# Kernel tuning notes

Hardware: AMD Instinct MI355X
Metric: run time of the kernel (lower is better)

The kernel has to match this reference:

```python
import jax, jax.numpy as jnp
import numpy as np

V, BLK, H, D, L = 32000, 1024, 16, 1024, 3
HD = D // H  # 64
B, T = 4, 1024


def _layernorm(x, g, b, eps=1e-5):
    mu = jnp.mean(x, axis=-1, keepdims=True)
    var = jnp.mean(jnp.square(x - mu), axis=-1, keepdims=True)
    return (x - mu) * jax.lax.rsqrt(var + eps) * g + b


def setup_inputs() -> dict:
    key = jax.random.key(0)
    ks = jax.random.split(key, 32)
    s = 0.02
    inp = {}
    inp["idx"] = jax.random.randint(ks[0], (B, T), 0, V)
    inp["target"] = jax.random.randint(ks[1], (B, T), 0, V)
    inp["tok_emb"] = jax.random.normal(ks[2], (V, D), jnp.float32) * s
    inp["pos_emb"] = jax.random.normal(ks[3], (BLK, D), jnp.float32) * s
    inp["wq"] = jax.random.normal(ks[4], (L, H, D, HD), jnp.float32) * s
    inp["wk"] = jax.random.normal(ks[5], (L, H, D, HD), jnp.float32) * s
    inp["wv"] = jax.random.normal(ks[6], (L, H, D, HD), jnp.float32) * s
    inp["wproj"] = jax.random.normal(ks[7], (L, D, D), jnp.float32) * s
    inp["bproj"] = jnp.zeros((L, D), jnp.float32)
    inp["ln1_g"] = jnp.ones((L, D), jnp.float32)
    inp["ln1_b"] = jnp.zeros((L, D), jnp.float32)
    inp["ln2_g"] = jnp.ones((L, D), jnp.float32)
    inp["ln2_b"] = jnp.zeros((L, D), jnp.float32)
    inp["w1"] = jax.random.normal(ks[8], (L, D, 4 * D), jnp.float32) * s
    inp["b1"] = jnp.zeros((L, 4 * D), jnp.float32)
    inp["w2"] = jax.random.normal(ks[9], (L, 4 * D, D), jnp.float32) * s
    inp["b2"] = jnp.zeros((L, D), jnp.float32)
    inp["lnf_g"] = jnp.ones((D,), jnp.float32)
    inp["lnf_b"] = jnp.zeros((D,), jnp.float32)
    inp["wlm"] = jax.random.normal(ks[10], (D, V), jnp.float32) * s
    inp["blm"] = jnp.zeros((V,), jnp.float32)
    return inp


def reference(idx, target, tok_emb, pos_emb, wq, wk, wv, wproj, bproj,
              ln1_g, ln1_b, ln2_g, ln2_b, w1, b1, w2, b2,
              lnf_g, lnf_b, wlm, blm):
    Bb, Tt = idx.shape
    x = tok_emb[idx] + pos_emb[:Tt]  # [B,T,D]
    mask = jnp.tril(jnp.ones((Tt, Tt), dtype=bool))  # causal
    scale = D ** -0.5  # NOTE: source scales by n_embd**-0.5, not head_size**-0.5
    for l in range(L):
        xn = _layernorm(x, ln1_g[l], ln1_b[l])
        q = jnp.einsum('btd,hde->bhte', xn, wq[l])
        k = jnp.einsum('btd,hde->bhte', xn, wk[l])
        v = jnp.einsum('btd,hde->bhte', xn, wv[l])
        scores = jnp.einsum('bhte,bhse->bhts', q, k) * scale
        scores = jnp.where(mask, scores, -jnp.inf)
        attn = jax.nn.softmax(scores, axis=-1)
        o = jnp.einsum('bhts,bhse->bhte', attn, v)
        o = o.transpose(0, 2, 1, 3).reshape(Bb, Tt, D)  # concat heads
        x = x + o @ wproj[l] + bproj[l]
        xn2 = _layernorm(x, ln2_g[l], ln2_b[l])
        h = jax.nn.relu(xn2 @ w1[l] + b1[l])
        x = x + h @ w2[l] + b2[l]
    x = _layernorm(x, lnf_g, lnf_b)
    logits = x @ wlm + blm  # [B,T,V]
    logp = jax.nn.log_softmax(logits, axis=-1)
    nll = -jnp.take_along_axis(logp, target[..., None], axis=-1)[..., 0]
    loss = jnp.mean(nll)
    return logits, loss
```

## Files before the change

kernel.cpp:

```cpp
#include <hip/hip_runtime.h>
#include <math.h>

#define Dn   1024
#define Hn   16
#define HDn  64
#define Tn   1024
#define Bn   4
#define Vn   32000
#define Ln   3
#define NT   (Bn*Tn)

typedef __attribute__((ext_vector_type(8))) short bf16x8;
typedef __attribute__((ext_vector_type(4))) float f32x4;

__device__ __forceinline__ float b2f(unsigned short u) {
  union { float f; unsigned int i; } c; c.i = ((unsigned int)u) << 16; return c.f;
}
__device__ __forceinline__ unsigned short f2b(float f) {
  union { float f; unsigned int i; } c; c.f = f;
  unsigned int r = (c.i + 0x7FFFu + ((c.i >> 16) & 1u)) >> 16;
  return (unsigned short)r;
}

#define GLOAD_LDS16(g, l) __builtin_amdgcn_global_load_lds( \
    (const __attribute__((address_space(1))) void*)(g),     \
    (__attribute__((address_space(3))) void*)(l), 16, 0, 0)

#define SBAR()  __builtin_amdgcn_s_barrier()
#define SCHED() __builtin_amdgcn_sched_barrier(0)

__device__ __forceinline__ void xcd_swz(int& bx, int& by) {
  int gx = gridDim.x, nwg = gx * gridDim.y;
  int lin = by * gx + bx;
  int swz = (lin & 7) * (nwg >> 3) + (lin >> 3);
  bx = swz % gx; by = swz / gx;
}

__global__ __launch_bounds__(256) void embed_kernel(
    const int* __restrict__ idx, const float* __restrict__ tok,
    const float* __restrict__ pos, float* __restrict__ x) {
  int row = blockIdx.x;
  int t = row & (Tn - 1);
  int token = idx[row];
  const float4* tp = (const float4*)(tok + (size_t)token * Dn);
  const float4* pp = (const float4*)(pos + (size_t)t * Dn);
  float4* xp = (float4*)(x + (size_t)row * Dn);
  int i = threadIdx.x;
  float4 a = tp[i], b = pp[i];
  xp[i] = make_float4(a.x + b.x, a.y + b.y, a.z + b.z, a.w + b.w);
}

__global__ __launch_bounds__(256) void ln_kernel(
    const float* __restrict__ x, const float* __restrict__ g,
    const float* __restrict__ b, unsigned short* __restrict__ y) {
  int row = blockIdx.x;
  const float4* xr = (const float4*)(x + (size_t)row * Dn);
  __shared__ float red[4];
  int lane = threadIdx.x & 63, w = threadIdx.x >> 6;

  float4 v = xr[threadIdx.x];
  float s = v.x + v.y + v.z + v.w;
  #pragma unroll
  for (int o = 32; o > 0; o >>= 1) s += __shfl_down(s, o, 64);
  if (lane == 0) red[w] = s;
  __syncthreads();
  float mu = (red[0] + red[1] + red[2] + red[3]) * (1.0f / Dn);
  __syncthreads();

  float dx = v.x - mu, dy = v.y - mu, dz = v.z - mu, dw = v.w - mu;
  float ss = dx*dx + dy*dy + dz*dz + dw*dw;
  #pragma unroll
  for (int o = 32; o > 0; o >>= 1) ss += __shfl_down(ss, o, 64);
  if (lane == 0) red[w] = ss;
  __syncthreads();
  float var = (red[0] + red[1] + red[2] + red[3]) * (1.0f / Dn);
  float inv = rsqrtf(var + 1e-5f);

  float4 gv = ((const float4*)g)[threadIdx.x];
  float4 bv = ((const float4*)b)[threadIdx.x];
  ushort4 o4;
  o4.x = f2b(dx*inv*gv.x + bv.x);
  o4.y = f2b(dy*inv*gv.y + bv.y);
  o4.z = f2b(dz*inv*gv.z + bv.z);
  o4.w = f2b(dw*inv*gv.w + bv.w);
  ((ushort4*)(y + (size_t)row * Dn))[threadIdx.x] = o4;
}

__global__ __launch_bounds__(256) void wcast_kernel(
    const float* __restrict__ src, unsigned short* __restrict__ dst,
    int K, int M, long long bsk, long long bsh) {
  __shared__ float t[32][33];
  int m0 = blockIdx.x << 5, k0 = blockIdx.y << 5;
  int tid = threadIdx.x;
  int ml = tid & 31, kl = tid >> 5;
  #pragma unroll
  for (int p = 0; p < 4; ++p) {
    int k = k0 + kl + p * 8;
    int m = m0 + ml;
    t[ml][kl + p * 8] = src[(size_t)k * bsk + (size_t)(m >> 6) * bsh + (m & 63)];
  }
  __syncthreads();
  int kl2 = tid & 31, ml2 = tid >> 5;
  #pragma unroll
  for (int p = 0; p < 4; ++p) {
    int m = m0 + ml2 + p * 8;
    int k = k0 + kl2;
    dst[(size_t)m * K + k] = f2b(t[ml2 + p * 8][kl2]);
  }
}

__global__ __launch_bounds__(256) void wcast3_kernel(
    const float* __restrict__ s0, const float* __restrict__ s1,
    const float* __restrict__ s2, unsigned short* __restrict__ dst) {
  const float* src = (blockIdx.z == 0) ? s0 : (blockIdx.z == 1) ? s1 : s2;
  unsigned short* d = dst + (size_t)blockIdx.z * 1024 * Dn;
  __shared__ float t[32][33];
  int m0 = blockIdx.x << 5, k0 = blockIdx.y << 5;
  int tid = threadIdx.x;
  int ml = tid & 31, kl = tid >> 5;
  #pragma unroll
  for (int p = 0; p < 4; ++p) {
    int k = k0 + kl + p * 8;
    int m = m0 + ml;
    t[ml][kl + p * 8] = src[(size_t)k * HDn + (size_t)(m >> 6) * (Dn * HDn) + (m & 63)];
  }
  __syncthreads();
  int kl2 = tid & 31, ml2 = tid >> 5;
  #pragma unroll
  for (int p = 0; p < 4; ++p) {
    int m = m0 + ml2 + p * 8;
    int k = k0 + kl2;
    d[(size_t)m * Dn + k] = f2b(t[ml2 + p * 8][kl2]);
  }
}

__global__ __launch_bounds__(512) void mm_bf16(
    const unsigned short* __restrict__ A, const unsigned short* __restrict__ BT,
    const float* __restrict__ bias, const float* __restrict__ res,
    float* __restrict__ Cf, unsigned short* __restrict__ Ch,
    int N, int K, int M, int relu) {
  __shared__ __align__(16) unsigned short As[3][128 * 32];
  __shared__ __align__(16) unsigned short Bs[3][128 * 32];
  const int tid = threadIdx.x;
  const int lane = tid & 63, w = tid >> 6, g = lane >> 4;
  const int wr = w >> 2, wc = w & 3;
  int bx = blockIdx.x, by = blockIdx.y;
  xcd_swz(bx, by);
  const int n0 = bx << 7, m0 = by << 7;

  f32x4 acc[4][2];
  #pragma unroll
  for (int i = 0; i < 4; ++i)
    #pragma unroll
    for (int j = 0; j < 2; ++j)
      acc[i][j] = (f32x4){0.f, 0.f, 0.f, 0.f};

  const int srow = tid >> 2, su = tid & 3;
  const int sks = su ^ ((srow >> 1) & 3);
  const unsigned short* a_g = A + (size_t)(n0 + srow) * K + sks * 8;
  const unsigned short* b_g = BT + (size_t)(m0 + srow) * K + sks * 8;

  int a_off[4], b_off[2];
  #pragma unroll
  for (int f = 0; f < 4; ++f) {
    int row = wr * 64 + f * 16 + (lane & 15);
    a_off[f] = row * 64 + ((g ^ ((row >> 1) & 3)) << 4);
  }
  #pragma unroll
  for (int f = 0; f < 2; ++f) {
    int col = wc * 32 + f * 16 + (lane & 15);
    b_off[f] = col * 64 + ((g ^ ((col >> 1) & 3)) << 4);
  }

#define MM_STAGE(buf, kk) do {                                   \
    GLOAD_LDS16(a_g + (kk), As[buf] + tid * 8);                  \
    GLOAD_LDS16(b_g + (kk), Bs[buf] + tid * 8); } while (0)

#define MM_COMPUTE(buf) do {                                     \
    bf16x8 af[4], bfr[2];                                        \
    _Pragma("unroll")                                            \
    for (int f = 0; f < 4; ++f)                                  \
      af[f] = *(const bf16x8*)((const char*)As[buf] + a_off[f]); \
    _Pragma("unroll")                                            \
    for (int f = 0; f < 2; ++f)                                  \
      bfr[f] = *(const bf16x8*)((const char*)Bs[buf] + b_off[f]);\
    _Pragma("unroll")                                            \
    for (int i = 0; i < 4; ++i)                                  \
      _Pragma("unroll")                                          \
      for (int j = 0; j < 2; ++j)                                \
        acc[i][j] = __builtin_amdgcn_mfma_f32_16x16x32_bf16(af[i], bfr[j], acc[i][j], 0, 0, 0); } while (0)

  MM_STAGE(0, 0);
  MM_STAGE(1, 32);
  int bc = 0, bp = 2;
  for (int k0 = 0; k0 < K; k0 += 32) {
    if (k0 + 32 < K) asm volatile("s_waitcnt vmcnt(2)" ::: "memory");
    else             asm volatile("s_waitcnt vmcnt(0)" ::: "memory");
    SCHED(); SBAR(); SCHED();
    if (k0 + 64 < K) MM_STAGE(bp, k0 + 64);
    MM_COMPUTE(bc);
    bc = (bc == 2) ? 0 : bc + 1;
    bp = (bp == 2) ? 0 : bp + 1;
  }

  #pragma unroll
  for (int fc = 0; fc < 2; ++fc) {
    int colg = m0 + wc * 32 + fc * 16 + (lane & 15);
    float bz = bias ? bias[colg] : 0.f;
    #pragma unroll
    for (int fr = 0; fr < 4; ++fr) {
      #pragma unroll
      for (int i = 0; i < 4; ++i) {
        int rowg = n0 + wr * 64 + fr * 16 + (g << 2) + i;
        float v = acc[fr][fc][i] + bz;
        if (res) v += res[(size_t)rowg * M + colg];
        if (relu) v = fmaxf(v, 0.f);
        if (Cf) Cf[(size_t)rowg * M + colg] = v;
        else    Ch[(size_t)rowg * M + colg] = f2b(v);
      }
    }
  }
#undef MM_STAGE
#undef MM_COMPUTE
}

template<int OMODE>
__global__ __launch_bounds__(512, 2) void mm256_bf16(
    const unsigned short* __restrict__ A, const unsigned short* __restrict__ BT,
    const float* __restrict__ bias, const float* __restrict__ res,
    float* __restrict__ Cf, unsigned short* __restrict__ Ch,
    float* __restrict__ rowsum, int N, int K, int M, int relu) {
  __shared__ __align__(16) unsigned short As[2][256 * 64];
  __shared__ __align__(16) unsigned short Bs[2][256 * 64];
  __shared__ float rsum2[OMODE == 4 ? 256 * 4 : 4];
  const int tid = threadIdx.x;
  const int lane = tid & 63, w = tid >> 6, g = lane >> 4;
  const int wr = w >> 2, wc = w & 3;
  int bx = blockIdx.x, by = blockIdx.y;
  xcd_swz(bx, by);
  const int n0 = bx << 8, m0 = by << 8;

  f32x4 acc[8][4];
  #pragma unroll
  for (int i = 0; i < 8; ++i)
    #pragma unroll
    for (int j = 0; j < 4; ++j)
      acc[i][j] = (f32x4){0.f, 0.f, 0.f, 0.f};

  const unsigned short* ag[4];
  const unsigned short* bg[4];
  int lofs[4];
  #pragma unroll
  for (int j = 0; j < 4; ++j) {
    int c = tid + 512 * j;
    int row = c >> 3, u = c & 7;
    int ks = u ^ (row & 7);
    ag[j] = A + (size_t)(n0 + row) * K + ks * 8;
    bg[j] = BT + (size_t)(m0 + row) * K + ks * 8;
    lofs[j] = c * 8;
  }

  int aoff[2][2][4], boff[2][2][2];
  #pragma unroll
  for (int h0 = 0; h0 < 2; ++h0)
    #pragma unroll
    for (int ks = 0; ks < 2; ++ks) {
      #pragma unroll
      for (int fr = 0; fr < 4; ++fr) {
        int r = wr * 128 + h0 * 64 + fr * 16 + (lane & 15);
        aoff[h0][ks][fr] = r * 128 + (((g + ks * 4) ^ (r & 7)) << 4);
      }
      #pragma unroll
      for (int fb = 0; fb < 2; ++fb) {
        int cB = wc * 64 + ks * 32 + fb * 16 + (lane & 15);
        (void)cB;
      }
    }
  #pragma unroll
  for (int h1 = 0; h1 < 2; ++h1)
    #pragma unroll
    for (int ks = 0; ks < 2; ++ks)
      #pragma unroll
      for (int fb = 0; fb < 2; ++fb) {
        int cB = wc * 64 + h1 * 32 + fb * 16 + (lane & 15);
        boff[h1][ks][fb] = cB * 128 + (((g + ks * 4) ^ (cB & 7)) << 4);
      }

  #pragma unroll
  for (int j = 0; j < 4; ++j) {
    GLOAD_LDS16(ag[j], As[0] + lofs[j]);
    GLOAD_LDS16(bg[j], Bs[0] + lofs[j]);
  }
  asm volatile("s_waitcnt vmcnt(0)" ::: "memory");
  SCHED(); SBAR(); SCHED();

  int cur = 0;
  const int NKT = K >> 6;
  for (int kt = 0; kt < NKT; ++kt) {
    if (kt + 1 < NKT) {
      const int kn = (kt + 1) << 6;
      #pragma unroll
      for (int j = 0; j < 4; ++j) {
        GLOAD_LDS16(ag[j] + kn, As[cur ^ 1] + lofs[j]);
        GLOAD_LDS16(bg[j] + kn, Bs[cur ^ 1] + lofs[j]);
      }
    }
    const char* Ab = (const char*)As[cur];
    const char* Bb = (const char*)Bs[cur];
    #pragma unroll
    for (int h0 = 0; h0 < 2; ++h0) {
      #pragma unroll
      for (int ks = 0; ks < 2; ++ks) {
        bf16x8 af[4];
        #pragma unroll
        for (int fr = 0; fr < 4; ++fr)
          af[fr] = *(const bf16x8*)(Ab + aoff[h0][ks][fr]);
        #pragma unroll
        for (int h1 = 0; h1 < 2; ++h1) {
          bf16x8 b0 = *(const bf16x8*)(Bb + boff[h1][ks][0]);
          bf16x8 b1 = *(const bf16x8*)(Bb + boff[h1][ks][1]);
          #pragma unroll
          for (int fr = 0; fr < 4; ++fr) {
            acc[h0 * 4 + fr][h1 * 2 + 0] =
                __builtin_amdgcn_mfma_f32_16x16x32_bf16(af[fr], b0, acc[h0 * 4 + fr][h1 * 2 + 0], 0, 0, 0);
            acc[h0 * 4 + fr][h1 * 2 + 1] =
                __builtin_amdgcn_mfma_f32_16x16x32_bf16(af[fr], b1, acc[h0 * 4 + fr][h1 * 2 + 1], 0, 0, 0);
          }
        }
      }
    }
    asm volatile("s_waitcnt vmcnt(0)" ::: "memory");
    SCHED(); SBAR(); SCHED();
    cur ^= 1;
  }

  if (OMODE == 0) {
    #pragma unroll
    for (int fc = 0; fc < 4; ++fc) {
      int colg = m0 + wc * 64 + fc * 16 + (lane & 15);
      float bz = bias ? bias[colg] : 0.f;
      #pragma unroll
      for (int fr = 0; fr < 8; ++fr) {
        #pragma unroll
        for (int i = 0; i < 4; ++i) {
          int rowg = n0 + wr * 128 + fr * 16 + (g << 2) + i;
          float v = acc[fr][fc][i] + bz;
          if (res) v += res[(size_t)rowg * M + colg];
          if (relu) v = fmaxf(v, 0.f);
          if (Cf) Cf[(size_t)rowg * M + colg] = v;
          else    Ch[(size_t)rowg * M + colg] = f2b(v);
        }
      }
    }
  } else if (OMODE == 3) {
    unsigned short* kb  = Ch + (size_t)NT * Dn;
    unsigned short* vtb = Ch + 2 * (size_t)NT * Dn;
    #pragma unroll
    for (int fc = 0; fc < 4; ++fc) {
      int colg = m0 + wc * 64 + fc * 16 + (lane & 15);
      int sel = colg >> 10, hh = (colg >> 6) & 15, e = colg & 63;
      #pragma unroll
      for (int fr = 0; fr < 8; ++fr) {
        int rowg0 = n0 + wr * 128 + fr * 16 + (g << 2);
        int b = rowg0 >> 10, t0 = rowg0 & 1023;
        if (sel == 2) {
          ushort4 pk;
          pk.x = f2b(acc[fr][fc][0]); pk.y = f2b(acc[fr][fc][1]);
          pk.z = f2b(acc[fr][fc][2]); pk.w = f2b(acc[fr][fc][3]);
          *(ushort4*)&vtb[(((size_t)(b * 16 + hh) * 64) + e) * 1024 + t0] = pk;
        } else {
          unsigned short* dst = (sel == 0) ? Ch : kb;
          #pragma unroll
          for (int i = 0; i < 4; ++i)
            dst[(((size_t)(b * 16 + hh) * 1024) + t0 + i) * 64 + e] = f2b(acc[fr][fc][i]);
        }
      }
    }
  } else {
    #pragma unroll
    for (int fr = 0; fr < 8; ++fr) {
      #pragma unroll
      for (int i = 0; i < 4; ++i) {
        int rloc = wr * 128 + fr * 16 + (g << 2) + i;
        int rowg = n0 + rloc;
        float es = 0.f;
        #pragma unroll
        for (int fc = 0; fc < 4; ++fc) {
          int colg = m0 + wc * 64 + fc * 16 + (lane & 15);
          float v = acc[fr][fc][i] + bias[colg];
          __builtin_nontemporal_store(v, &Cf[(size_t)rowg * M + colg]);
          es += __expf(v);
        }
        es += __shfl_xor(es, 1); es += __shfl_xor(es, 2);
        es += __shfl_xor(es, 4); es += __shfl_xor(es, 8);
        if ((lane & 15) == 0) rsum2[rloc * 4 + wc] = es;
      }
    }
    __syncthreads();
    if (tid < 256)
      atomicAdd(&rowsum[n0 + tid],
                rsum2[tid * 4 + 0] + rsum2[tid * 4 + 1] +
                rsum2[tid * 4 + 2] + rsum2[tid * 4 + 3]);
  }
}

__global__ __launch_bounds__(256) void fattn_kernel(
    const unsigned short* __restrict__ qg, const unsigned short* __restrict__ kg,
    const unsigned short* __restrict__ vtg, unsigned short* __restrict__ ob) {
  const int bid = blockIdx.x;
  const int qt = bid & 15, bh = bid >> 4;
  const int b = bh >> 4, h = bh & 15;
  const int tid = threadIdx.x, lane = tid & 63, w = tid >> 6, g = lane >> 4;

  __shared__ __align__(16) unsigned short Ks[2][64 * 64];
  __shared__ __align__(16) unsigned short Vs[2][64 * 64];
  __shared__ __align__(16) unsigned short Pb[4][16 * 64];

  const unsigned short* kbase = kg + (size_t)bh * Tn * HDn;
  const unsigned short* vbase = vtg + (size_t)bh * HDn * Tn;

  const int qrow = qt * 64 + w * 16 + (lane & 15);
  const unsigned short* qptr = qg + ((size_t)bh * Tn + qrow) * HDn;
  bf16x8 qf0 = *(const bf16x8*)(qptr + g * 8);
  bf16x8 qf1 = *(const bf16x8*)(qptr + 32 + g * 8);

  f32x4 accO[4];
  #pragma unroll
  for (int dt = 0; dt < 4; ++dt) accO[dt] = (f32x4){0.f, 0.f, 0.f, 0.f};
  float mrun[4] = {-1e30f, -1e30f, -1e30f, -1e30f};
  float lrun[4] = {0.f, 0.f, 0.f, 0.f};

  const float scale = 0.03125f;
  const int qout0 = qt * 64 + w * 16 + 4 * g;

  unsigned short* pb = &Pb[w][0];
  const int nsteps = qt + 1;

#define FA_STAGE(buf, s0_) do {                                              \
    _Pragma("unroll")                                                        \
    for (int r = 0; r < 2; ++r) {                                            \
      int c = tid + 256 * r;                                                 \
      int srow = c >> 3, u = c & 7;                                          \
      GLOAD_LDS16(kbase + (size_t)((s0_) + srow) * HDn + ((u ^ (srow & 7)) * 8), Ks[buf] + c * 8); \
    }                                                                        \
    _Pragma("unroll")                                                        \
    for (int r = 0; r < 2; ++r) {                                            \
      int c = tid + 256 * r;                                                 \
      int d = c >> 3, u = c & 7;                                             \
      GLOAD_LDS16(vbase + (size_t)d * Tn + (s0_) + ((u ^ (d & 7)) * 8), Vs[buf] + c * 8); \
    } } while (0)

  FA_STAGE(0, 0);
  int cur = 0;

  for (int st = 0; st < nsteps; ++st) {
    const int s0 = st * 64;
    if (st + 1 < nsteps) {
      FA_STAGE(cur ^ 1, s0 + 64);
      asm volatile("s_waitcnt vmcnt(4)" ::: "memory");
    } else {
      asm volatile("s_waitcnt vmcnt(0)" ::: "memory");
    }
    SCHED(); SBAR(); SCHED();

    float p[4][4];
    #pragma unroll
    for (int sub = 0; sub < 4; ++sub) {
      int srow = sub * 16 + (lane & 15);
      const char* kr = (const char*)Ks[cur] + srow * 128;
      bf16x8 kf0 = *(const bf16x8*)(kr + ((g ^ (srow & 7)) * 16));
      bf16x8 kf1 = *(const bf16x8*)(kr + (((4 + g) ^ (srow & 7)) * 16));
      f32x4 s4 = (f32x4){0.f, 0.f, 0.f, 0.f};
      s4 = __builtin_amdgcn_mfma_f32_16x16x32_bf16(qf0, kf0, s4, 0, 0, 0);
      s4 = __builtin_amdgcn_mfma_f32_16x16x32_bf16(qf1, kf1, s4, 0, 0, 0);
      int sg = s0 + srow;
      #pragma unroll
      for (int i = 0; i < 4; ++i)
        p[sub][i] = (sg > qout0 + i) ? -1e30f : s4[i] * scale;
    }

    #pragma unroll
    for (int i = 0; i < 4; ++i) {
      float v = fmaxf(fmaxf(p[0][i], p[1][i]), fmaxf(p[2][i], p[3][i]));
      v = fmaxf(v, __shfl_xor(v, 1)); v = fmaxf(v, __shfl_xor(v, 2));
      v = fmaxf(v, __shfl_xor(v, 4)); v = fmaxf(v, __shfl_xor(v, 8));
      float nm = fmaxf(mrun[i], v);
      float fac = __expf(mrun[i] - nm);
      mrun[i] = nm;
      #pragma unroll
      for (int dt = 0; dt < 4; ++dt) accO[dt][i] *= fac;
      float sum = 0.f;
      #pragma unroll
      for (int sub = 0; sub < 4; ++sub) {
        float e = __expf(p[sub][i] - nm);
        p[sub][i] = e;
        sum += e;
      }
      sum += __shfl_xor(sum, 1); sum += __shfl_xor(sum, 2);
      sum += __shfl_xor(sum, 4); sum += __shfl_xor(sum, 8);
      lrun[i] = lrun[i] * fac + sum;
    }

    #pragma unroll
    for (int sub = 0; sub < 4; ++sub) {
      int s = sub * 16 + (lane & 15);
      #pragma unroll
      for (int i = 0; i < 4; ++i) {
        int q = 4 * g + i;
        pb[q * 64 + (((s >> 3) ^ (q & 7)) * 8) + (s & 7)] = f2b(p[sub][i]);
      }
    }

    #pragma unroll
    for (int sc = 0; sc < 2; ++sc) {
      int qq = lane & 15;
      bf16x8 pa = *(const bf16x8*)((const char*)pb + qq * 128 + (((sc * 4 + g) ^ (qq & 7)) * 16));
      #pragma unroll
      for (int dt = 0; dt < 4; ++dt) {
        int d = dt * 16 + (lane & 15);
        bf16x8 vf = *(const bf16x8*)((const char*)Vs[cur] + d * 128 + (((sc * 4 + g) ^ (d & 7)) * 16));
        accO[dt] = __builtin_amdgcn_mfma_f32_16x16x32_bf16(pa, vf, accO[dt], 0, 0, 0);
      }
    }

    SCHED(); SBAR(); SCHED();
    cur ^= 1;
  }
#undef FA_STAGE

  float rinv[4];
  #pragma unroll
  for (int i = 0; i < 4; ++i) rinv[i] = 1.0f / lrun[i];
  #pragma unroll
  for (int dt = 0; dt < 4; ++dt) {
    int dcol = h * 64 + dt * 16 + (lane & 15);
    #pragma unroll
    for (int i = 0; i < 4; ++i) {
      int t = qout0 + i;
      ob[((size_t)(b * Tn + t)) * Dn + dcol] = f2b(accO[dt][i] * rinv[i]);
    }
  }
}

__global__ __launch_bounds__(256) void loss_kernel(
    const float* __restrict__ logits, const float* __restrict__ rowsum,
    const int* __restrict__ target, float* __restrict__ out_loss) {
  __shared__ float red[4];
  int lane = threadIdx.x & 63, w = threadIdx.x >> 6;
  float s = 0.f;
  for (int row = threadIdx.x; row < NT; row += 256) {
    float lt = logits[(size_t)row * Vn + target[row]];
    s += logf(rowsum[row]) - lt;
  }
  #pragma unroll
  for (int off = 32; off > 0; off >>= 1) s += __shfl_down(s, off, 64);
  if (lane == 0) red[w] = s;
  __syncthreads();
  if (threadIdx.x == 0)
    *out_loss = (red[0] + red[1] + red[2] + red[3]) * (1.0f / NT);
}

static inline void launch_wcast(const float* src, unsigned short* dst, int K, int M,
                                long long bsk, long long bsh, hipStream_t s) {
  dim3 g(M >> 5, K >> 5);
  wcast_kernel<<<g, 256, 0, s>>>(src, dst, K, M, bsk, bsh);
}

static inline void launch_mm(const unsigned short* A, const unsigned short* BT,
                             const float* bias, const float* res,
                             float* Cf, unsigned short* Ch,
                             int N, int K, int M, int relu, hipStream_t s) {
  dim3 g(N >> 7, M >> 7);
  mm_bf16<<<g, 512, 0, s>>>(A, BT, bias, res, Cf, Ch, N, K, M, relu);
}

template<int OMODE>
static inline void launch_mm256(const unsigned short* A, const unsigned short* BT,
                                const float* bias, const float* res,
                                float* Cf, unsigned short* Ch, float* rowsum,
                                int N, int K, int M, int relu, hipStream_t s) {
  dim3 g(N >> 8, M >> 8);
  mm256_bf16<OMODE><<<g, 512, 0, s>>>(A, BT, bias, res, Cf, Ch, rowsum, N, K, M, relu);
}

extern "C" void kernel_launch(void* const* d_in, const int* in_sizes, int n_in,
                              void* d_out, int out_size, void* d_ws, size_t ws_size,
                              hipStream_t stream) {
  const int*   idx    = (const int*)d_in[0];
  const int*   target = (const int*)d_in[1];
  const float* tok    = (const float*)d_in[2];
  const float* pos    = (const float*)d_in[3];
  const float* wq     = (const float*)d_in[4];
  const float* wk     = (const float*)d_in[5];
  const float* wv     = (const float*)d_in[6];
  const float* wproj  = (const float*)d_in[7];
  const float* bproj  = (const float*)d_in[8];
  const float* ln1g   = (const float*)d_in[9];
  const float* ln1b   = (const float*)d_in[10];
  const float* ln2g   = (const float*)d_in[11];
  const float* ln2b   = (const float*)d_in[12];
  const float* w1     = (const float*)d_in[13];
  const float* b1     = (const float*)d_in[14];
  const float* w2     = (const float*)d_in[15];
  const float* b2     = (const float*)d_in[16];
  const float* lnfg   = (const float*)d_in[17];
  const float* lnfb   = (const float*)d_in[18];
  const float* wlm    = (const float*)d_in[19];
  const float* blm    = (const float*)d_in[20];

  float* out = (float*)d_out;

  char* p = (char*)d_ws;
  float* x  = (float*)p;                 p += (size_t)NT * Dn * 4;
  unsigned short* xn = (unsigned short*)p; p += (size_t)NT * Dn * 2;
  unsigned short* reg = (unsigned short*)p; p += (size_t)NT * 4 * Dn * 2;
  unsigned short* wT = (unsigned short*)p; p += (size_t)Vn * Dn * 2;
  float* rowsum = (float*)p;

  unsigned short* qb  = reg;
  unsigned short* kb  = reg + (size_t)NT * Dn;
  unsigned short* vtb = reg + 2 * (size_t)NT * Dn;
  unsigned short* ob  = reg + 3 * (size_t)NT * Dn;
  unsigned short* hb  = reg;

  embed_kernel<<<NT, 256, 0, stream>>>(idx, tok, pos, x);

  for (int l = 0; l < Ln; ++l) {
    const float* wq_l = wq + (size_t)l * Hn * Dn * HDn;
    const float* wk_l = wk + (size_t)l * Hn * Dn * HDn;
    const float* wv_l = wv + (size_t)l * Hn * Dn * HDn;

    ln_kernel<<<NT, 256, 0, stream>>>(x, ln1g + l * Dn, ln1b + l * Dn, xn);

    {
      dim3 g3(32, 32, 3);
      wcast3_kernel<<<g3, 256, 0, stream>>>(wq_l, wk_l, wv_l, wT);
    }
    launch_mm256<3>(xn, wT, nullptr, nullptr, nullptr, qb, nullptr, NT, Dn, 3072, 0, stream);

    fattn_kernel<<<Bn * Hn * (Tn / 64), 256, 0, stream>>>(qb, kb, vtb, ob);

    launch_wcast(wproj + (size_t)l * Dn * Dn, wT, Dn, Dn, Dn, 64, stream);
    launch_mm(ob, wT, bproj + l * Dn, x, x, nullptr, NT, Dn, Dn, 0, stream);

    ln_kernel<<<NT, 256, 0, stream>>>(x, ln2g + l * Dn, ln2b + l * Dn, xn);

    launch_wcast(w1 + (size_t)l * Dn * 4 * Dn, wT, Dn, 4 * Dn, 4 * Dn, 64, stream);
    launch_mm256<0>(xn, wT, b1 + l * 4 * Dn, nullptr, nullptr, hb, nullptr, NT, Dn, 4 * Dn, 1, stream);
    launch_wcast(w2 + (size_t)l * 4 * Dn * Dn, wT, 4 * Dn, Dn, Dn, 64, stream);
    launch_mm(hb, wT, b2 + l * Dn, x, x, nullptr, NT, 4 * Dn, Dn, 0, stream);
  }

  ln_kernel<<<NT, 256, 0, stream>>>(x, lnfg, lnfb, xn);

  hipMemsetAsync(rowsum, 0, NT * sizeof(float), stream);
  launch_wcast(wlm, wT, Dn, Vn, Vn, 64, stream);
  launch_mm256<4>(xn, wT, blm, nullptr, out, nullptr, rowsum, NT, Dn, Vn, 0, stream);

  loss_kernel<<<1, 256, 0, stream>>>(out, rowsum, target, out + (size_t)NT * Vn);
}
```

Measured before the change: 1.279 ms.

## Restructure 256x256 GEMM main loop into four-phase staggered A/B prefetch pipeline

Splits the 256x256 bf16 GEMM's LDS tiles into 128-row halves and reorders the K loop into four MFMA phases, each separated by a barrier. A tiles are prefetched two iterations ahead and B tiles one ahead, with a partial vmcnt wait instead of a full drain. MFMA phases run at raised wave priority via s_setprio. Launch bounds drop to one block per CU, which frees registers for the extra fragment buffers but gives up a second resident block to hide latency.

```diff
diff --git a/kernel.cpp b/kernel.cpp
--- a/kernel.cpp
+++ b/kernel.cpp
@@ -225,13 +225,13 @@
 }
 
 template<int OMODE>
-__global__ __launch_bounds__(512, 2) void mm256_bf16(
+__global__ __launch_bounds__(512, 1) void mm256_bf16(
     const unsigned short* __restrict__ A, const unsigned short* __restrict__ BT,
     const float* __restrict__ bias, const float* __restrict__ res,
     float* __restrict__ Cf, unsigned short* __restrict__ Ch,
     float* __restrict__ rowsum, int N, int K, int M, int relu) {
-  __shared__ __align__(16) unsigned short As[2][256 * 64];
-  __shared__ __align__(16) unsigned short Bs[2][256 * 64];
+  __shared__ __align__(16) unsigned short Ah[2][2][128 * 64];
+  __shared__ __align__(16) unsigned short Bh[2][2][128 * 64];
   __shared__ float rsum2[OMODE == 4 ? 256 * 4 : 4];
   const int tid = threadIdx.x;
   const int lane = tid & 63, w = tid >> 6, g = lane >> 4;
@@ -247,92 +247,111 @@
     for (int j = 0; j < 4; ++j)
       acc[i][j] = (f32x4){0.f, 0.f, 0.f, 0.f};
 
-  const unsigned short* ag[4];
-  const unsigned short* bg[4];
-  int lofs[4];
-  #pragma unroll
-  for (int j = 0; j < 4; ++j) {
-    int c = tid + 512 * j;
-    int row = c >> 3, u = c & 7;
-    int ks = u ^ (row & 7);
-    ag[j] = A + (size_t)(n0 + row) * K + ks * 8;
-    bg[j] = BT + (size_t)(m0 + row) * K + ks * 8;
-    lofs[j] = c * 8;
-  }
+  const int c0 = tid, c1 = tid + 512;
+  const int r0 = c0 >> 3, s0 = (c0 & 7) ^ (r0 & 7);
+  const int r1 = c1 >> 3, s1 = (c1 & 7) ^ (r1 & 7);
+  const int l0 = c0 * 8, l1 = c1 * 8;
+  const unsigned short* agp[2][2];
+  const unsigned short* bgp[2][2];
+  #pragma unroll
+  for (int h = 0; h < 2; ++h) {
+    agp[h][0] = A  + (size_t)(n0 + h * 128 + r0) * K + s0 * 8;
+    agp[h][1] = A  + (size_t)(n0 + h * 128 + r1) * K + s1 * 8;
+    bgp[h][0] = BT + (size_t)(m0 + h * 128 + r0) * K + s0 * 8;
+    bgp[h][1] = BT + (size_t)(m0 + h * 128 + r1) * K + s1 * 8;
+  }
+
+#define STA(h, d, kt) do {                                        \
+    GLOAD_LDS16(agp[h][0] + (size_t)(kt) * 64, &Ah[d][h][l0]);    \
+    GLOAD_LDS16(agp[h][1] + (size_t)(kt) * 64, &Ah[d][h][l1]); } while (0)
+#define STB(h, d, kt) do {                                        \
+    GLOAD_LDS16(bgp[h][0] + (size_t)(kt) * 64, &Bh[d][h][l0]);    \
+    GLOAD_LDS16(bgp[h][1] + (size_t)(kt) * 64, &Bh[d][h][l1]); } while (0)
 
   int aoff[2][2][4], boff[2][2][2];
   #pragma unroll
   for (int h0 = 0; h0 < 2; ++h0)
     #pragma unroll
-    for (int ks = 0; ks < 2; ++ks) {
+    for (int ks = 0; ks < 2; ++ks)
       #pragma unroll
       for (int fr = 0; fr < 4; ++fr) {
-        int r = wr * 128 + h0 * 64 + fr * 16 + (lane & 15);
-        aoff[h0][ks][fr] = r * 128 + (((g + ks * 4) ^ (r & 7)) << 4);
-      }
+        int rh = h0 * 64 + fr * 16 + (lane & 15);
+        aoff[h0][ks][fr] = rh * 128 + (((ks * 4 + g) ^ (rh & 7)) << 4);
+      }
+  #pragma unroll
+  for (int hc = 0; hc < 2; ++hc)
+    #pragma unroll
+    for (int ks = 0; ks < 2; ++ks)
       #pragma unroll
       for (int fb = 0; fb < 2; ++fb) {
-        int cB = wc * 64 + ks * 32 + fb * 16 + (lane & 15);
-        (void)cB;
-      }
-    }
-  #pragma unroll
-  for (int h1 = 0; h1 < 2; ++h1)
-    #pragma unroll
-    for (int ks = 0; ks < 2; ++ks)
-      #pragma unroll
-      for (int fb = 0; fb < 2; ++fb) {
-        int cB = wc * 64 + h1 * 32 + fb * 16 + (lane & 15);
-        boff[h1][ks][fb] = cB * 128 + (((g + ks * 4) ^ (cB & 7)) << 4);
-      }
-
-  #pragma unroll
-  for (int j = 0; j < 4; ++j) {
-    GLOAD_LDS16(ag[j], As[0] + lofs[j]);
-    GLOAD_LDS16(bg[j], Bs[0] + lofs[j]);
-  }
-  asm volatile("s_waitcnt vmcnt(0)" ::: "memory");
-  SCHED(); SBAR(); SCHED();
-
-  int cur = 0;
+        int ch = (wc & 1) * 64 + (hc * 2 + fb) * 16 + (lane & 15);
+        boff[hc][ks][fb] = ch * 128 + (((ks * 4 + g) ^ (ch & 7)) << 4);
+      }
+
+#define LOAD_A(H0) do {                                           \
+    _Pragma("unroll")                                             \
+    for (int ks = 0; ks < 2; ++ks)                                \
+      _Pragma("unroll")                                           \
+      for (int fr = 0; fr < 4; ++fr)                              \
+        af[ks][fr] = *(const bf16x8*)(Ab + aoff[H0][ks][fr]); } while (0)
+#define LOAD_B(HC) do {                                           \
+    _Pragma("unroll")                                             \
+    for (int ks = 0; ks < 2; ++ks)                                \
+      _Pragma("unroll")                                           \
+      for (int fb = 0; fb < 2; ++fb)                              \
+        bf[ks][fb] = *(const bf16x8*)(Bb + boff[HC][ks][fb]); } while (0)
+#define PH_MFMA(H0, HC) do {                                      \
+    __builtin_amdgcn_s_setprio(1);                                \
+    _Pragma("unroll")                                             \
+    for (int ks = 0; ks < 2; ++ks)                                \
+      _Pragma("unroll")                                           \
+      for (int fr = 0; fr < 4; ++fr)                              \
+        _Pragma("unroll")                                         \
+        for (int fb = 0; fb < 2; ++fb)                            \
+          acc[(H0) * 4 + fr][(HC) * 2 + fb] =                     \
+            __builtin_amdgcn_mfma_f32_16x16x32_bf16(af[ks][fr], bf[ks][fb], \
+                acc[(H0) * 4 + fr][(HC) * 2 + fb], 0, 0, 0);      \
+    __builtin_amdgcn_s_setprio(0); } while (0)
+#define LGKM0() do { asm volatile("s_waitcnt lgkmcnt(0)" ::: "memory"); SCHED(); } while (0)
+
   const int NKT = K >> 6;
+  STA(0, 0, 0); STA(1, 0, 0);
+  STB(0, 0, 0); STB(1, 0, 0);
+  if (NKT > 1) { STA(0, 1, 1); STA(1, 1, 1); }
+
   for (int kt = 0; kt < NKT; ++kt) {
-    if (kt + 1 < NKT) {
-      const int kn = (kt + 1) << 6;
-      #pragma unroll
-      for (int j = 0; j < 4; ++j) {
-        GLOAD_LDS16(ag[j] + kn, As[cur ^ 1] + lofs[j]);
-        GLOAD_LDS16(bg[j] + kn, Bs[cur ^ 1] + lofs[j]);
-      }
-    }
-    const char* Ab = (const char*)As[cur];
-    const char* Bb = (const char*)Bs[cur];
-    #pragma unroll
-    for (int h0 = 0; h0 < 2; ++h0) {
-      #pragma unroll
-      for (int ks = 0; ks < 2; ++ks) {
-        bf16x8 af[4];
-        #pragma unroll
-        for (int fr = 0; fr < 4; ++fr)
-          af[fr] = *(const bf16x8*)(Ab + aoff[h0][ks][fr]);
-        #pragma unroll
-        for (int h1 = 0; h1 < 2; ++h1) {
-          bf16x8 b0 = *(const bf16x8*)(Bb + boff[h1][ks][0]);
-          bf16x8 b1 = *(const bf16x8*)(Bb + boff[h1][ks][1]);
-          #pragma unroll
-          for (int fr = 0; fr < 4; ++fr) {
-            acc[h0 * 4 + fr][h1 * 2 + 0] =
-                __builtin_amdgcn_mfma_f32_16x16x32_bf16(af[fr], b0, acc[h0 * 4 + fr][h1 * 2 + 0], 0, 0, 0);
-            acc[h0 * 4 + fr][h1 * 2 + 1] =
-                __builtin_amdgcn_mfma_f32_16x16x32_bf16(af[fr], b1, acc[h0 * 4 + fr][h1 * 2 + 1], 0, 0, 0);
-          }
-        }
-      }
-    }
-    asm volatile("s_waitcnt vmcnt(0)" ::: "memory");
-    SCHED(); SBAR(); SCHED();
-    cur ^= 1;
-  }
+    const int d = kt & 1;
+    const char* Ab = (const char*)&Ah[d][wr][0];
+    const char* Bb = (const char*)&Bh[d][wc >> 1][0];
+    bf16x8 af[2][4], bf[2][2];
+    if (kt + 1 < NKT) { STB(0, (kt + 1) & 1, kt + 1); STB(1, (kt + 1) & 1, kt + 1); }
+    if (kt + 1 < NKT) asm volatile("s_waitcnt vmcnt(8)" ::: "memory");
+    else              asm volatile("s_waitcnt vmcnt(0)" ::: "memory");
+    SCHED(); SBAR(); SCHED();
+    LOAD_A(0); LOAD_B(0);
+    LGKM0();
+    PH_MFMA(0, 0);
+    SCHED(); SBAR(); SCHED();
+    LOAD_B(1);
+    LGKM0();
+    PH_MFMA(0, 1);
+    SCHED(); SBAR(); SCHED();
+    LOAD_A(1);
+    LGKM0();
+    PH_MFMA(1, 1);
+    SCHED(); SBAR(); SCHED();
+    LOAD_B(0);
+    if (kt + 2 < NKT) { STA(0, d, kt + 2); STA(1, d, kt + 2); }
+    LGKM0();
+    PH_MFMA(1, 0);
+    SCHED(); SBAR(); SCHED();
+  }
+#undef STA
+#undef STB
+#undef LOAD_A
+#undef LOAD_B
+#undef PH_MFMA
+#undef LGKM0
 
   if (OMODE == 0) {
     #pragma unroll
```

New measurement: 1.296 ms. Within noise of the previous version (+1.3%).
